# Optimization experiments

Measured on AMD Instinct MI355X. Metric: run time of the kernel, lower is better.

The kernel has to match this reference:

```python
import jax, jax.numpy as jnp
import numpy as np

BINS = 10
LOSS_WEIGHT = 1.0


def setup_inputs() -> dict:
    key = jax.random.key(0)
    k1, k2, k3 = jax.random.split(key, 3)
    N, C = 262144, 80
    pred = jax.random.normal(k1, (N, C), dtype=jnp.float32)
    # binary class targets (sparse positives, as in detection)
    target = (jax.random.uniform(k2, (N, C)) < 0.02).astype(jnp.float32)
    # 1 = valid sample, 0 = ignored
    label_weight = (jax.random.uniform(k3, (N, C)) < 0.95).astype(jnp.float32)
    return {"pred": pred, "target": target, "label_weight": label_weight}


def reference(pred, target, label_weight):
    # GHM-C loss, momentum=0 path (no EMA buffer).
    valid = label_weight > 0
    validf = valid.astype(jnp.float32)
    tot = jnp.maximum(jnp.sum(validf), 1.0)

    # gradient norm g = |sigmoid(pred).detach() - target|, in [0, 1]
    g = jnp.abs(jax.lax.stop_gradient(jax.nn.sigmoid(pred)) - target)
    # edges are i/BINS with last edge 1+1e-6, so bin i covers [i/B, (i+1)/B);
    # equivalent to floor(g*B) clipped to [0, B-1] (g==1 lands in last bin).
    bin_idx = jnp.clip(jnp.floor(g * BINS).astype(jnp.int32), 0, BINS - 1)

    # per-bin counts over valid elements (single-pass histogram)
    counts = jax.ops.segment_sum(validf.reshape(-1), bin_idx.reshape(-1),
                                 num_segments=BINS)
    n = jnp.sum(counts > 0).astype(jnp.float32)  # number of non-empty bins
    per_bin_w = jnp.where(counts > 0, tot / jnp.maximum(counts, 1.0), 0.0)
    weights = per_bin_w[bin_idx] * validf  # scattered weight assignment
    weights = jnp.where(n > 0, weights / n, weights)

    # binary_cross_entropy_with_logits, elementwise: softplus(x) - x*t
    bce = jax.nn.softplus(pred) - pred * target
    loss = jnp.sum(bce * weights) / tot
    return loss * LOSS_WEIGHT
```

## Files before the change

kernel.cpp:

```cpp
#include <hip/hip_runtime.h>

#define BINS 10


__device__ __forceinline__ void ghmc_elem(float pk, float tk, float wk,
                                          float* __restrict__ S,
                                          float* __restrict__ C,
                                          const float* __restrict__ T) {
    float m  = fmaf(-2.0f, tk, 1.0f);
    float q  = m * pk;
    bool  valid = wk > 0.0f;
    float qm = valid ? q : -1.0e30f;
    float u  = __expf(-fabsf(q));
    float bce = fmaxf(q, 0.0f) + __logf(1.0f + u);
    float bw  = bce * wk;
    S[0] += bw;
    C[0] += valid ? 1.0f : 0.0f;
#pragma unroll
    for (int j = 0; j < 9; ++j) {
        bool pr = qm >= T[j];
        S[j + 1] += pr ? bw : 0.0f;
        C[j + 1] += pr ? 1.0f : 0.0f;
    }
}

__device__ __forceinline__ void ghmc_vec4(float4 p, float4 t, float4 w,
                                          float* S, float* C, const float* T) {
    const float* pp = (const float*)&p;
    const float* tt = (const float*)&t;
    const float* ww = (const float*)&w;
#pragma unroll
    for (int e = 0; e < 4; ++e) ghmc_elem(pp[e], tt[e], ww[e], S, C, T);
}

__global__ __launch_bounds__(256) void ghmc_main(
    const float* __restrict__ pred, const float* __restrict__ targ,
    const float* __restrict__ lw, float* __restrict__ part, int n, int grid) {

    const float T[9] = {-2.19722458f, -1.38629436f, -0.84729786f, -0.40546511f,
                        0.0f, 0.40546511f, 0.84729786f, 1.38629436f, 2.19722458f};

    float S[BINS], C[BINS];
#pragma unroll
    for (int k = 0; k < BINS; ++k) { S[k] = 0.0f; C[k] = 0.0f; }

    const int tid    = blockIdx.x * blockDim.x + threadIdx.x;
    const int stride = grid * blockDim.x;
    const int nvec   = n >> 2;

    const float4* p4 = (const float4*)pred;
    const float4* t4 = (const float4*)targ;
    const float4* w4 = (const float4*)lw;

    int i = tid;
    for (; i + stride < nvec; i += 2 * stride) {
        const int i2 = i + stride;
        float4 pA = p4[i],  tA = t4[i],  wA = w4[i];
        float4 pB = p4[i2], tB = t4[i2], wB = w4[i2];
        ghmc_vec4(pA, tA, wA, S, C, T);
        ghmc_vec4(pB, tB, wB, S, C, T);
    }
    for (; i < nvec; i += stride) ghmc_vec4(p4[i], t4[i], w4[i], S, C, T);
    {
        int rem = n & 3;
        if (tid < rem) {
            int idx = (nvec << 2) + tid;
            ghmc_elem(pred[idx], targ[idx], lw[idx], S, C, T);
        }
    }

    __shared__ float sS[BINS];
    __shared__ float sC[BINS];
    if (threadIdx.x < BINS) { sS[threadIdx.x] = 0.0f; sC[threadIdx.x] = 0.0f; }
    __syncthreads();

    const int lane = threadIdx.x & 63;
#pragma unroll
    for (int k = 0; k < BINS; ++k) {
        float s = S[k], c = C[k];
#pragma unroll
        for (int off = 32; off > 0; off >>= 1) {
            s += __shfl_xor(s, off, 64);
            c += __shfl_xor(c, off, 64);
        }
        if (lane == 0) { atomicAdd(&sS[k], s); atomicAdd(&sC[k], c); }
    }
    __syncthreads();

    if (threadIdx.x < BINS) {
        part[threadIdx.x * grid + blockIdx.x]          = sS[threadIdx.x];
        part[(BINS + threadIdx.x) * grid + blockIdx.x] = sC[threadIdx.x];
    }
}

__global__ __launch_bounds__(256) void ghmc_fin(
    const float* __restrict__ part, float* __restrict__ out, int grid) {
    __shared__ float rows[2 * BINS];
    __shared__ float wsum[4];
    for (int k = 0; k < 2 * BINS; ++k) {
        float v = 0.0f;
        for (int i = threadIdx.x; i < grid; i += 256) v += part[k * grid + i];
#pragma unroll
        for (int off = 32; off > 0; off >>= 1) v += __shfl_xor(v, off, 64);
        if ((threadIdx.x & 63) == 0) wsum[threadIdx.x >> 6] = v;
        __syncthreads();
        if (threadIdx.x == 0) rows[k] = wsum[0] + wsum[1] + wsum[2] + wsum[3];
        __syncthreads();
    }
    if (threadIdx.x == 0) {
        float acc = 0.0f;
        int   nb  = 0;
#pragma unroll
        for (int b = 0; b < BINS; ++b) {
            float sN = (b < BINS - 1) ? rows[b + 1]        : 0.0f;
            float cN = (b < BINS - 1) ? rows[BINS + b + 1] : 0.0f;
            float s  = rows[b] - sN;
            float c  = rows[BINS + b] - cN;
            if (c > 0.5f) { nb += 1; acc += s / c; }
        }
        out[0] = (nb > 0) ? (acc / (float)nb) : 0.0f;
    }
}

extern "C" void kernel_launch(void* const* d_in, const int* in_sizes, int n_in,
                              void* d_out, int out_size, void* d_ws, size_t ws_size,
                              hipStream_t stream) {
    const float* pred = (const float*)d_in[0];
    const float* targ = (const float*)d_in[1];
    const float* lw   = (const float*)d_in[2];
    float* out  = (float*)d_out;
    float* part = (float*)d_ws;
    const int n = in_sizes[0];

    int grid = 2048;
    size_t need = (size_t)grid * 2 * BINS * sizeof(float);
    if (ws_size < need) {
        grid = (int)(ws_size / (2 * BINS * sizeof(float)));
        if (grid < 1) grid = 1;
    }

    ghmc_main<<<grid, 256, 0, stream>>>(pred, targ, lw, part, n, grid);
    ghmc_fin<<<1, 256, 0, stream>>>(part, out, grid);
}
```

Before: 291.1 us.

## Replace per-thread cumulative threshold histogram with shared-memory atomic bins

```diff
diff --git a/kernel.cpp b/kernel.cpp
--- a/kernel.cpp
+++ b/kernel.cpp
@@ -1,48 +1,36 @@
 #include <hip/hip_runtime.h>
 
 #define BINS 10
+#define NBUF 64
+#define BUFSTRIDE 21
 
 
 __device__ __forceinline__ void ghmc_elem(float pk, float tk, float wk,
-                                          float* __restrict__ S,
-                                          float* __restrict__ C,
-                                          const float* __restrict__ T) {
+                                          float* __restrict__ hb) {
+    const float NL2E = -1.44269504f;
     float m  = fmaf(-2.0f, tk, 1.0f);
     float q  = m * pk;
-    bool  valid = wk > 0.0f;
-    float qm = valid ? q : -1.0e30f;
+    float e2 = __expf(-q);
+    float g  = __builtin_amdgcn_rcpf(1.0f + e2);
+    int   bi = (int)(g * 10.0f);
+    bi = bi > (BINS - 1) ? (BINS - 1) : bi;
     float u  = __expf(-fabsf(q));
-    float bce = fmaxf(q, 0.0f) + __logf(1.0f + u);
-    float bw  = bce * wk;
-    S[0] += bw;
-    C[0] += valid ? 1.0f : 0.0f;
-#pragma unroll
-    for (int j = 0; j < 9; ++j) {
-        bool pr = qm >= T[j];
-        S[j + 1] += pr ? bw : 0.0f;
-        C[j + 1] += pr ? 1.0f : 0.0f;
-    }
-}
-
-__device__ __forceinline__ void ghmc_vec4(float4 p, float4 t, float4 w,
-                                          float* S, float* C, const float* T) {
-    const float* pp = (const float*)&p;
-    const float* tt = (const float*)&t;
-    const float* ww = (const float*)&w;
-#pragma unroll
-    for (int e = 0; e < 4; ++e) ghmc_elem(pp[e], tt[e], ww[e], S, C, T);
+    float bce = fmaf(__logf(1.0f + u), 1.0f, fmaxf(q, 0.0f));
+    atomicAdd(&hb[bi], bce * wk);
+    atomicAdd(&hb[bi + BINS], wk);
+    (void)NL2E;
 }
 
 __global__ __launch_bounds__(256) void ghmc_main(
     const float* __restrict__ pred, const float* __restrict__ targ,
     const float* __restrict__ lw, float* __restrict__ part, int n, int grid) {
 
-    const float T[9] = {-2.19722458f, -1.38629436f, -0.84729786f, -0.40546511f,
-                        0.0f, 0.40546511f, 0.84729786f, 1.38629436f, 2.19722458f};
+    __shared__ float h[NBUF * BUFSTRIDE];
+    for (int i = threadIdx.x; i < NBUF * BUFSTRIDE; i += 256) h[i] = 0.0f;
+    __syncthreads();
 
-    float S[BINS], C[BINS];
-#pragma unroll
-    for (int k = 0; k < BINS; ++k) { S[k] = 0.0f; C[k] = 0.0f; }
+    const int buf = ((threadIdx.x >> 6) << 4) | (threadIdx.x & 15);
+    float* hb = &h[buf * BUFSTRIDE];
 
     const int tid    = blockIdx.x * blockDim.x + threadIdx.x;
     const int stride = grid * blockDim.x;
@@ -57,39 +45,36 @@
         const int i2 = i + stride;
         float4 pA = p4[i],  tA = t4[i],  wA = w4[i];
         float4 pB = p4[i2], tB = t4[i2], wB = w4[i2];
-        ghmc_vec4(pA, tA, wA, S, C, T);
-        ghmc_vec4(pB, tB, wB, S, C, T);
+        ghmc_elem(pA.x, tA.x, wA.x, hb);
+        ghmc_elem(pA.y, tA.y, wA.y, hb);
+        ghmc_elem(pA.z, tA.z, wA.z, hb);
+        ghmc_elem(pA.w, tA.w, wA.w, hb);
+        ghmc_elem(pB.x, tB.x, wB.x, hb);
+        ghmc_elem(pB.y, tB.y, wB.y, hb);
+        ghmc_elem(pB.z, tB.z, wB.z, hb);
+        ghmc_elem(pB.w, tB.w, wB.w, hb);
     }
-    for (; i < nvec; i += stride) ghmc_vec4(p4[i], t4[i], w4[i], S, C, T);
+    for (; i < nvec; i += stride) {
+        float4 p = p4[i], t = t4[i], w = w4[i];
+        ghmc_elem(p.x, t.x, w.x, hb);
+        ghmc_elem(p.y, t.y, w.y, hb);
+        ghmc_elem(p.z, t.z, w.z, hb);
+        ghmc_elem(p.w, t.w, w.w, hb);
+    }
     {
         int rem = n & 3;
         if (tid < rem) {
             int idx = (nvec << 2) + tid;
-            ghmc_elem(pred[idx], targ[idx], lw[idx], S, C, T);
+            ghmc_elem(pred[idx], targ[idx], lw[idx], hb);
         }
     }
 
-    __shared__ float sS[BINS];
-    __shared__ float sC[BINS];
-    if (threadIdx.x < BINS) { sS[threadIdx.x] = 0.0f; sC[threadIdx.x] = 0.0f; }
     __syncthreads();
-
-    const int lane = threadIdx.x & 63;
-#pragma unroll
-    for (int k = 0; k < BINS; ++k) {
-        float s = S[k], c = C[k];
-#pragma unroll
-        for (int off = 32; off > 0; off >>= 1) {
-            s += __shfl_xor(s, off, 64);
-            c += __shfl_xor(c, off, 64);
-        }
-        if (lane == 0) { atomicAdd(&sS[k], s); atomicAdd(&sC[k], c); }
-    }
-    __syncthreads();
-
-    if (threadIdx.x < BINS) {
-        part[threadIdx.x * grid + blockIdx.x]          = sS[threadIdx.x];
-        part[(BINS + threadIdx.x) * grid + blockIdx.x] = sC[threadIdx.x];
+    if (threadIdx.x < 2 * BINS) {
+        float v = 0.0f;
+#pragma unroll 8
+        for (int k = 0; k < NBUF; ++k) v += h[k * BUFSTRIDE + threadIdx.x];
+        part[threadIdx.x * grid + blockIdx.x] = v;
     }
 }
 
@@ -112,10 +97,8 @@
         int   nb  = 0;
 #pragma unroll
         for (int b = 0; b < BINS; ++b) {
-            float sN = (b < BINS - 1) ? rows[b + 1]        : 0.0f;
-            float cN = (b < BINS - 1) ? rows[BINS + b + 1] : 0.0f;
-            float s  = rows[b] - sN;
-            float c  = rows[BINS + b] - cN;
+            float s = rows[b];
+            float c = rows[BINS + b];
             if (c > 0.5f) { nb += 1; acc += s / c; }
         }
         out[0] = (nb > 0) ? (acc / (float)nb) : 0.0f;
```

New measurement: 405.8 us. +39.4%, slower.
